# Kernel optimization log

Measured on AMD Instinct MI355X. Metric: run time of the kernel, lower is better.

The kernel has to match this reference:

```python
import jax, jax.numpy as jnp
import numpy as np

MAX_DEPTH = 10
NUM_INPUT = 256
NUM_OUTPUT = 64
BATCH = 131072
N_INTERNAL = 2**MAX_DEPTH - 1  # 1023 heap-indexed internal nodes
N_LEAVES = 2**MAX_DEPTH        # 1024 leaves


def setup_inputs() -> dict:
    key = jax.random.key(0)
    k_x, k_w, k_b, k_a, k_l = jax.random.split(key, 5)
    x = jax.random.normal(k_x, (BATCH, NUM_INPUT), dtype=jnp.float32)
    # internal-node params (torch init: weights ~ N(0,0.1); bias/alpha zeros,
    # but we randomize bias/alpha so both branches are exercised)
    W = jax.random.normal(k_w, (N_INTERNAL, NUM_INPUT), dtype=jnp.float32) * 0.1
    b = jax.random.normal(k_b, (N_INTERNAL,), dtype=jnp.float32) * 0.1
    alpha = jax.random.normal(k_a, (N_INTERNAL,), dtype=jnp.float32)
    leaves = jax.random.normal(k_l, (N_LEAVES, NUM_OUTPUT), dtype=jnp.float32)
    return {"x": x, "W": W, "b": b, "alpha": alpha, "leaves": leaves}


def reference(x, W, b, alpha, leaves):
    # Batched hard root-to-leaf traversal of the soft binary tree.
    # Heap indexing: node i -> left child 2i+1, right child 2i+2.
    B = x.shape[0]
    idx = jnp.zeros((B,), dtype=jnp.int32)
    mult = jnp.ones((B,), dtype=x.dtype)
    for _ in range(MAX_DEPTH):  # fixed small structural loop over depth levels
        w = W[idx]  # [B, F] gather of per-node weights
        val = jax.nn.sigmoid(alpha[idx] * (jnp.einsum('bf,bf->b', x, w) + b[idx]))
        go_right = val >= 0.5
        # right branch contributes val, left branch contributes (1 - val)
        mult = mult * jnp.where(go_right, val, 1.0 - val)
        idx = 2 * idx + 1 + go_right.astype(jnp.int32)
    leaf_idx = idx - N_INTERNAL  # [B]
    return mult[:, None] * leaves[leaf_idx]  # [B, num_output]
```

## Files before the change

kernel.cpp:

```cpp
#include <hip/hip_runtime.h>

#define NUM_INPUT   256
#define NUM_OUTPUT  64
#define MAX_DEPTH   10
#define N_INTERNAL  1023
#define STAGED_NODES 31
#define THREADS 512
#define NBLOCKS 1024
#define ELEMS_PER_GROUP 4

__device__ __forceinline__ float group16_reduce_add(float acc) {
    int t;
    t = __builtin_amdgcn_update_dpp(0, __float_as_int(acc), 0x121, 0xf, 0xf, true);
    acc += __int_as_float(t);
    t = __builtin_amdgcn_update_dpp(0, __float_as_int(acc), 0x122, 0xf, 0xf, true);
    acc += __int_as_float(t);
    t = __builtin_amdgcn_update_dpp(0, __float_as_int(acc), 0x124, 0xf, 0xf, true);
    acc += __int_as_float(t);
    t = __builtin_amdgcn_update_dpp(0, __float_as_int(acc), 0x128, 0xf, 0xf, true);
    acc += __int_as_float(t);
    return acc;
}

__device__ __forceinline__ float group16_reduce_mul(float v) {
    int t;
    t = __builtin_amdgcn_update_dpp(0, __float_as_int(v), 0x121, 0xf, 0xf, true);
    v *= __int_as_float(t);
    t = __builtin_amdgcn_update_dpp(0, __float_as_int(v), 0x122, 0xf, 0xf, true);
    v *= __int_as_float(t);
    t = __builtin_amdgcn_update_dpp(0, __float_as_int(v), 0x124, 0xf, 0xf, true);
    v *= __int_as_float(t);
    t = __builtin_amdgcn_update_dpp(0, __float_as_int(v), 0x128, 0xf, 0xf, true);
    v *= __int_as_float(t);
    return v;
}

#define STEP_X(BASE, IDX, ZND, X0, X1, X2, X3)                              \
    {                                                                       \
        float a_i = lds_a[IDX];                                             \
        float b_i = lds_b[IDX];                                             \
        const float4* wr_ = reinterpret_cast<const float4*>(                \
            (BASE) + (size_t)(IDX) * NUM_INPUT);                            \
        float4 w0 = wr_[s], w1 = wr_[16 + s], w2 = wr_[32 + s], w3 = wr_[48 + s]; \
        float a0 = X0.x * w0.x, a1 = X1.x * w1.x;                           \
        float a2 = X2.x * w2.x, a3 = X3.x * w3.x;                           \
        a0 = fmaf(X0.y, w0.y, a0); a1 = fmaf(X1.y, w1.y, a1);               \
        a2 = fmaf(X2.y, w2.y, a2); a3 = fmaf(X3.y, w3.y, a3);               \
        a0 = fmaf(X0.z, w0.z, a0); a1 = fmaf(X1.z, w1.z, a1);               \
        a2 = fmaf(X2.z, w2.z, a2); a3 = fmaf(X3.z, w3.z, a3);               \
        a0 = fmaf(X0.w, w0.w, a0); a1 = fmaf(X1.w, w1.w, a1);               \
        a2 = fmaf(X2.w, w2.w, a2); a3 = fmaf(X3.w, w3.w, a3);               \
        float acc_ = group16_reduce_add((a0 + a1) + (a2 + a3));             \
        float z = a_i * (acc_ + b_i);                                       \
        ZND = __int_as_float(__float_as_int(z) | 0x80000000);               \
        IDX = 2 * (IDX) + 1 + ((z >= 0.0f) ? 1 : 0);                        \
    }

#define ONE_ELEM(E, XC0, XC1, XC2, XC3, XN0, XN1, XN2, XN3, PF)             \
    {                                                                       \
        int idx = 0;                                                        \
        float zn0, zn1, zn2, zn3, zn4, zn5, zn6, zn7, zn8, zn9;             \
                                        \
        STEP_X(lds_w, idx, zn0, XC0, XC1, XC2, XC3)                         \
        STEP_X(lds_w, idx, zn1, XC0, XC1, XC2, XC3)                         \
        STEP_X(lds_w, idx, zn2, XC0, XC1, XC2, XC3)                         \
        STEP_X(lds_w, idx, zn3, XC0, XC1, XC2, XC3)                         \
        STEP_X(lds_w, idx, zn4, XC0, XC1, XC2, XC3)                         \
        if (PF) {                                                           \
            const float4* xp_ = reinterpret_cast<const float4*>(            \
                x + (size_t)(gbase + 4 * ((E) + 1)) * NUM_INPUT);           \
            XN0 = xp_[s];      XN1 = xp_[16 + s];                           \
            XN2 = xp_[32 + s]; XN3 = xp_[48 + s];                           \
            __builtin_amdgcn_sched_barrier(0);                              \
        }                                                                   \
           \
        STEP_X(W, idx, zn5, XC0, XC1, XC2, XC3)                             \
        STEP_X(W, idx, zn6, XC0, XC1, XC2, XC3)                             \
        STEP_X(W, idx, zn7, XC0, XC1, XC2, XC3)                             \
        STEP_X(W, idx, zn8, XC0, XC1, XC2, XC3)                             \
        STEP_X(W, idx, zn9, XC0, XC1, XC2, XC3)                             \
                 \
        float zsel = -1e30f;                                                \
        zsel = (s == 0) ? zn0 : zsel; zsel = (s == 1) ? zn1 : zsel;         \
        zsel = (s == 2) ? zn2 : zsel; zsel = (s == 3) ? zn3 : zsel;         \
        zsel = (s == 4) ? zn4 : zsel; zsel = (s == 5) ? zn5 : zsel;         \
        zsel = (s == 6) ? zn6 : zsel; zsel = (s == 7) ? zn7 : zsel;         \
        zsel = (s == 8) ? zn8 : zsel; zsel = (s == 9) ? zn9 : zsel;         \
        float f = 1.0f + __expf(zsel);                                      \
        float p = group16_reduce_mul(f);                                    \
        float mult = 1.0f / p;                                              \
        const int leaf = idx - N_INTERNAL;                                  \
        const float4 lv = reinterpret_cast<const float4*>(                  \
            leaves + (size_t)leaf * NUM_OUTPUT)[s];                         \
        float4 o;                                                           \
        o.x = mult * lv.x; o.y = mult * lv.y;                               \
        o.z = mult * lv.z; o.w = mult * lv.w;                               \
        reinterpret_cast<float4*>(                                          \
            out + (size_t)(gbase + 4 * (E)) * NUM_OUTPUT)[s] = o;           \
    }

__global__ __launch_bounds__(THREADS, 4) void ogtree_kernel(
    const float* __restrict__ x,
    const float* __restrict__ W,
    const float* __restrict__ b,
    const float* __restrict__ alpha,
    const float* __restrict__ leaves,
    float* __restrict__ out)
{
    __shared__ float lds_w[STAGED_NODES * NUM_INPUT];
    __shared__ float lds_b[N_INTERNAL];
    __shared__ float lds_a[N_INTERNAL];

    const int tid  = threadIdx.x;
    const int lane = tid & 63;
    const int wid  = tid >> 6;
    const int g    = lane >> 4;
    const int s    = lane & 15;
    const int gbase = blockIdx.x * (THREADS / 64) * 16 + wid * 16 + g;

    const float4* xp0 = reinterpret_cast<const float4*>(x + (size_t)gbase * NUM_INPUT);
    float4 xa0 = xp0[s], xa1 = xp0[16 + s], xa2 = xp0[32 + s], xa3 = xp0[48 + s];

    {
        const float4* Wv = reinterpret_cast<const float4*>(W);
        float4* lw4 = reinterpret_cast<float4*>(lds_w);
        #pragma unroll
        for (int i = tid; i < STAGED_NODES * NUM_INPUT / 4; i += THREADS)
            lw4[i] = Wv[i];
        for (int i = tid; i < N_INTERNAL; i += THREADS) {
            lds_b[i] = b[i];
            lds_a[i] = alpha[i];
        }
    }
    __syncthreads();

    float4 xb0, xb1, xb2, xb3;

    ONE_ELEM(0, xa0, xa1, xa2, xa3, xb0, xb1, xb2, xb3, 1)
    ONE_ELEM(1, xb0, xb1, xb2, xb3, xa0, xa1, xa2, xa3, 1)
    ONE_ELEM(2, xa0, xa1, xa2, xa3, xb0, xb1, xb2, xb3, 1)
    ONE_ELEM(3, xb0, xb1, xb2, xb3, xa0, xa1, xa2, xa3, 0)
}

extern "C" void kernel_launch(void* const* d_in, const int* in_sizes, int n_in,
                              void* d_out, int out_size, void* d_ws, size_t ws_size,
                              hipStream_t stream) {
    const float* x      = (const float*)d_in[0];
    const float* W      = (const float*)d_in[1];
    const float* b      = (const float*)d_in[2];
    const float* alpha  = (const float*)d_in[3];
    const float* leaves = (const float*)d_in[4];
    float* out = (float*)d_out;

    ogtree_kernel<<<NBLOCKS, THREADS, 0, stream>>>(x, W, b, alpha, leaves, out);
}
```

Measured before the change: 47.14 us.

## Software-pipeline global-W tree levels of one element with LDS levels of the next

Restructures the per-wave loop over four batch elements so that the five deep tree levels of element E, whose weights come from global memory, are interleaved with the five shallow LDS-staged levels of element E+1. Each global weight row load is issued before an independent LDS step, so the dependent global latency is partly hidden. x rows are triple-buffered and prefetched one element further ahead. The cost is higher register pressure from the extra x buffer and two live sets of z values, which may reduce occupancy under the 4-block launch bound.

```diff
diff --git a/kernel.cpp b/kernel.cpp
--- a/kernel.cpp
+++ b/kernel.cpp
@@ -2,12 +2,10 @@
 
 #define NUM_INPUT   256
 #define NUM_OUTPUT  64
-#define MAX_DEPTH   10
 #define N_INTERNAL  1023
 #define STAGED_NODES 31
 #define THREADS 512
 #define NBLOCKS 1024
-#define ELEMS_PER_GROUP 4
 
 __device__ __forceinline__ float group16_reduce_add(float acc) {
     int t;
@@ -35,12 +33,20 @@
     return v;
 }
 
-#define STEP_X(BASE, IDX, ZND, X0, X1, X2, X3)                              \
+#define XISSUE(E, X0, X1, X2, X3)                                           \
+    {                                                                       \
+        const float4* xp_ = reinterpret_cast<const float4*>(                \
+            x + (size_t)(gbase + 4 * (E)) * NUM_INPUT);                     \
+        X0 = xp_[s]; X1 = xp_[16 + s]; X2 = xp_[32 + s]; X3 = xp_[48 + s];  \
+        __builtin_amdgcn_sched_barrier(0);                                  \
+    }
+
+#define LSTEP(IDX, ZND, X0, X1, X2, X3)                                     \
     {                                                                       \
         float a_i = lds_a[IDX];                                             \
         float b_i = lds_b[IDX];                                             \
         const float4* wr_ = reinterpret_cast<const float4*>(                \
-            (BASE) + (size_t)(IDX) * NUM_INPUT);                            \
+            lds_w + (size_t)(IDX) * NUM_INPUT);                             \
         float4 w0 = wr_[s], w1 = wr_[16 + s], w2 = wr_[32 + s], w3 = wr_[48 + s]; \
         float a0 = X0.x * w0.x, a1 = X1.x * w1.x;                           \
         float a2 = X2.x * w2.x, a3 = X3.x * w3.x;                           \
@@ -56,40 +62,60 @@
         IDX = 2 * (IDX) + 1 + ((z >= 0.0f) ? 1 : 0);                        \
     }
 
-#define ONE_ELEM(E, XC0, XC1, XC2, XC3, XN0, XN1, XN2, XN3, PF)             \
-    {                                                                       \
-        int idx = 0;                                                        \
-        float zn0, zn1, zn2, zn3, zn4, zn5, zn6, zn7, zn8, zn9;             \
-                                        \
-        STEP_X(lds_w, idx, zn0, XC0, XC1, XC2, XC3)                         \
-        STEP_X(lds_w, idx, zn1, XC0, XC1, XC2, XC3)                         \
-        STEP_X(lds_w, idx, zn2, XC0, XC1, XC2, XC3)                         \
-        STEP_X(lds_w, idx, zn3, XC0, XC1, XC2, XC3)                         \
-        STEP_X(lds_w, idx, zn4, XC0, XC1, XC2, XC3)                         \
-        if (PF) {                                                           \
-            const float4* xp_ = reinterpret_cast<const float4*>(            \
-                x + (size_t)(gbase + 4 * ((E) + 1)) * NUM_INPUT);           \
-            XN0 = xp_[s];      XN1 = xp_[16 + s];                           \
-            XN2 = xp_[32 + s]; XN3 = xp_[48 + s];                           \
-            __builtin_amdgcn_sched_barrier(0);                              \
-        }                                                                   \
-           \
-        STEP_X(W, idx, zn5, XC0, XC1, XC2, XC3)                             \
-        STEP_X(W, idx, zn6, XC0, XC1, XC2, XC3)                             \
-        STEP_X(W, idx, zn7, XC0, XC1, XC2, XC3)                             \
-        STEP_X(W, idx, zn8, XC0, XC1, XC2, XC3)                             \
-        STEP_X(W, idx, zn9, XC0, XC1, XC2, XC3)                             \
-                 \
+#define DISSUE(IDX)                                                         \
+    {                                                                       \
+        const float4* wr_ = reinterpret_cast<const float4*>(                \
+            W + (size_t)(IDX) * NUM_INPUT);                                 \
+        wd0 = wr_[s]; wd1 = wr_[16 + s]; wd2 = wr_[32 + s]; wd3 = wr_[48 + s]; \
+    }
+#define DCONSUME(IDX, ZND, X0, X1, X2, X3)                                  \
+    {                                                                       \
+        float a_i = lds_a[IDX];                                             \
+        float b_i = lds_b[IDX];                                             \
+        float a0 = X0.x * wd0.x, a1 = X1.x * wd1.x;                         \
+        float a2 = X2.x * wd2.x, a3 = X3.x * wd3.x;                         \
+        a0 = fmaf(X0.y, wd0.y, a0); a1 = fmaf(X1.y, wd1.y, a1);             \
+        a2 = fmaf(X2.y, wd2.y, a2); a3 = fmaf(X3.y, wd3.y, a3);             \
+        a0 = fmaf(X0.z, wd0.z, a0); a1 = fmaf(X1.z, wd1.z, a1);             \
+        a2 = fmaf(X2.z, wd2.z, a2); a3 = fmaf(X3.z, wd3.z, a3);             \
+        a0 = fmaf(X0.w, wd0.w, a0); a1 = fmaf(X1.w, wd1.w, a1);             \
+        a2 = fmaf(X2.w, wd2.w, a2); a3 = fmaf(X3.w, wd3.w, a3);             \
+        float acc_ = group16_reduce_add((a0 + a1) + (a2 + a3));             \
+        float z = a_i * (acc_ + b_i);                                       \
+        ZND = __int_as_float(__float_as_int(z) | 0x80000000);               \
+        IDX = 2 * (IDX) + 1 + ((z >= 0.0f) ? 1 : 0);                        \
+    }
+
+#define DL_TICK(IDXD, IDXL, ZD5, ZD6, ZD7, ZD8, ZD9, ZL0, ZL1, ZL2, ZL3, ZL4, \
+                XD0, XD1, XD2, XD3, XL0, XL1, XL2, XL3)                     \
+    DISSUE(IDXD)                                                            \
+    LSTEP(IDXL, ZL0, XL0, XL1, XL2, XL3)                                    \
+    DCONSUME(IDXD, ZD5, XD0, XD1, XD2, XD3)                                 \
+    DISSUE(IDXD)                                                            \
+    LSTEP(IDXL, ZL1, XL0, XL1, XL2, XL3)                                    \
+    DCONSUME(IDXD, ZD6, XD0, XD1, XD2, XD3)                                 \
+    DISSUE(IDXD)                                                            \
+    LSTEP(IDXL, ZL2, XL0, XL1, XL2, XL3)                                    \
+    DCONSUME(IDXD, ZD7, XD0, XD1, XD2, XD3)                                 \
+    DISSUE(IDXD)                                                            \
+    LSTEP(IDXL, ZL3, XL0, XL1, XL2, XL3)                                    \
+    DCONSUME(IDXD, ZD8, XD0, XD1, XD2, XD3)                                 \
+    DISSUE(IDXD)                                                            \
+    LSTEP(IDXL, ZL4, XL0, XL1, XL2, XL3)                                    \
+    DCONSUME(IDXD, ZD9, XD0, XD1, XD2, XD3)
+
+#define EPI(E, IDX, Z0, Z1, Z2, Z3, Z4, Z5, Z6, Z7, Z8, Z9)                 \
+    {                                                                       \
         float zsel = -1e30f;                                                \
-        zsel = (s == 0) ? zn0 : zsel; zsel = (s == 1) ? zn1 : zsel;         \
-        zsel = (s == 2) ? zn2 : zsel; zsel = (s == 3) ? zn3 : zsel;         \
-        zsel = (s == 4) ? zn4 : zsel; zsel = (s == 5) ? zn5 : zsel;         \
-        zsel = (s == 6) ? zn6 : zsel; zsel = (s == 7) ? zn7 : zsel;         \
-        zsel = (s == 8) ? zn8 : zsel; zsel = (s == 9) ? zn9 : zsel;         \
+        zsel = (s == 0) ? Z0 : zsel; zsel = (s == 1) ? Z1 : zsel;           \
+        zsel = (s == 2) ? Z2 : zsel; zsel = (s == 3) ? Z3 : zsel;           \
+        zsel = (s == 4) ? Z4 : zsel; zsel = (s == 5) ? Z5 : zsel;           \
+        zsel = (s == 6) ? Z6 : zsel; zsel = (s == 7) ? Z7 : zsel;           \
+        zsel = (s == 8) ? Z8 : zsel; zsel = (s == 9) ? Z9 : zsel;           \
         float f = 1.0f + __expf(zsel);                                      \
         float p = group16_reduce_mul(f);                                    \
         float mult = 1.0f / p;                                              \
-        const int leaf = idx - N_INTERNAL;                                  \
+        const int leaf = (IDX) - N_INTERNAL;                                \
         const float4 lv = reinterpret_cast<const float4*>(                  \
             leaves + (size_t)leaf * NUM_OUTPUT)[s];                         \
         float4 o;                                                           \
@@ -118,8 +144,11 @@
     const int s    = lane & 15;
     const int gbase = blockIdx.x * (THREADS / 64) * 16 + wid * 16 + g;
 
-    const float4* xp0 = reinterpret_cast<const float4*>(x + (size_t)gbase * NUM_INPUT);
-    float4 xa0 = xp0[s], xa1 = xp0[16 + s], xa2 = xp0[32 + s], xa3 = xp0[48 + s];
+    float4 xa0, xa1, xa2, xa3;
+    float4 xb0, xb1, xb2, xb3;
+    float4 xc0, xc1, xc2, xc3;
+
+    XISSUE(0, xa0, xa1, xa2, xa3)
 
     {
         const float4* Wv = reinterpret_cast<const float4*>(W);
@@ -134,12 +163,47 @@
     }
     __syncthreads();
 
-    float4 xb0, xb1, xb2, xb3;
-
-    ONE_ELEM(0, xa0, xa1, xa2, xa3, xb0, xb1, xb2, xb3, 1)
-    ONE_ELEM(1, xb0, xb1, xb2, xb3, xa0, xa1, xa2, xa3, 1)
-    ONE_ELEM(2, xa0, xa1, xa2, xa3, xb0, xb1, xb2, xb3, 1)
-    ONE_ELEM(3, xb0, xb1, xb2, xb3, xa0, xa1, xa2, xa3, 0)
+    float ZA0, ZA1, ZA2, ZA3, ZA4, ZA5, ZA6, ZA7, ZA8, ZA9;
+    float ZB0, ZB1, ZB2, ZB3, ZB4, ZB5, ZB6, ZB7, ZB8, ZB9;
+    float4 wd0, wd1, wd2, wd3;
+    int idxA, idxB;
+
+    XISSUE(1, xb0, xb1, xb2, xb3)
+    idxA = 0;
+    LSTEP(idxA, ZA0, xa0, xa1, xa2, xa3)
+    LSTEP(idxA, ZA1, xa0, xa1, xa2, xa3)
+    LSTEP(idxA, ZA2, xa0, xa1, xa2, xa3)
+    LSTEP(idxA, ZA3, xa0, xa1, xa2, xa3)
+    LSTEP(idxA, ZA4, xa0, xa1, xa2, xa3)
+
+    XISSUE(2, xc0, xc1, xc2, xc3)
+    idxB = 0;
+    DL_TICK(idxA, idxB, ZA5, ZA6, ZA7, ZA8, ZA9, ZB0, ZB1, ZB2, ZB3, ZB4,
+            xa0, xa1, xa2, xa3, xb0, xb1, xb2, xb3)
+    EPI(0, idxA, ZA0, ZA1, ZA2, ZA3, ZA4, ZA5, ZA6, ZA7, ZA8, ZA9)
+
+    XISSUE(3, xa0, xa1, xa2, xa3)
+    idxA = 0;
+    DL_TICK(idxB, idxA, ZB5, ZB6, ZB7, ZB8, ZB9, ZA0, ZA1, ZA2, ZA3, ZA4,
+            xb0, xb1, xb2, xb3, xc0, xc1, xc2, xc3)
+    EPI(1, idxB, ZB0, ZB1, ZB2, ZB3, ZB4, ZB5, ZB6, ZB7, ZB8, ZB9)
+
+    idxB = 0;
+    DL_TICK(idxA, idxB, ZA5, ZA6, ZA7, ZA8, ZA9, ZB0, ZB1, ZB2, ZB3, ZB4,
+            xc0, xc1, xc2, xc3, xa0, xa1, xa2, xa3)
+    EPI(2, idxA, ZA0, ZA1, ZA2, ZA3, ZA4, ZA5, ZA6, ZA7, ZA8, ZA9)
+
+    DISSUE(idxB)
+    DCONSUME(idxB, ZB5, xa0, xa1, xa2, xa3)
+    DISSUE(idxB)
+    DCONSUME(idxB, ZB6, xa0, xa1, xa2, xa3)
+    DISSUE(idxB)
+    DCONSUME(idxB, ZB7, xa0, xa1, xa2, xa3)
+    DISSUE(idxB)
+    DCONSUME(idxB, ZB8, xa0, xa1, xa2, xa3)
+    DISSUE(idxB)
+    DCONSUME(idxB, ZB9, xa0, xa1, xa2, xa3)
+    EPI(3, idxB, ZB0, ZB1, ZB2, ZB3, ZB4, ZB5, ZB6, ZB7, ZB8, ZB9)
 }
 
 extern "C" void kernel_launch(void* const* d_in, const int* in_sizes, int n_in,
```

After: 49.84 us. +5.7%, slower.
